# Optimization experiments

Measured on AMD Instinct MI355X. Metric: run time of the kernel, lower is better.

Reference implementation:

```python
import jax, jax.numpy as jnp
import numpy as np

OUT_FEATURES = 4096
IN_FEATURES = 4096
R = 16
DIST = 4
N_FREQ = 10000
SCALING = 150.0


def setup_inputs() -> dict:
    key = jax.random.key(0)
    k_x, k_w, k_b, k_s, k_a, k_i = jax.random.split(key, 6)
    x = jax.random.normal(k_x, (4, 2048, IN_FEATURES), dtype=jnp.float32)
    base_w = jax.random.normal(k_w, (OUT_FEATURES, IN_FEATURES), dtype=jnp.float32) * 0.02
    base_b = jax.random.normal(k_b, (OUT_FEATURES,), dtype=jnp.float32) * 0.02
    spectrum = jax.random.normal(k_s, (N_FREQ,), dtype=jnp.float32)
    hora_A = jax.random.normal(k_a, (R, IN_FEATURES), dtype=jnp.float32)
    # torch uses randperm(r*out_features)[:n_frequency] -> unique flat indices
    idx = jax.random.permutation(k_i, R * OUT_FEATURES)[:N_FREQ].astype(jnp.int32)
    return {"x": x, "base_w": base_w, "base_b": base_b,
            "spectrum": spectrum, "hora_A": hora_A, "idx": idx}


def reference(x, base_w, base_b, spectrum, hora_A, idx):
    # --- get_delta_weight ---
    rows = idx // R            # index into out_features
    cols = idx % R             # index into r
    dense_spectrum = jnp.zeros((OUT_FEATURES, R), dtype=spectrum.dtype)
    dense_spectrum = dense_spectrum.at[rows, cols].set(spectrum)
    # chunk_size = ceil(out/dist) = 1024; out divisible by dist -> pure reshape
    chunks = dense_spectrum.reshape(DIST, OUT_FEATURES // DIST, R)
    B = jnp.fft.ifft2(chunks, axes=(-2, -1)).real.astype(spectrum.dtype)
    B = B.reshape(OUT_FEATURES, R)
    delta_w = (B * SCALING) @ hora_A          # [out_features, in_features]
    # --- forward: base linear + adapter linear ---
    base_out = jnp.einsum('bsi,oi->bso', x, base_w) + base_b
    result = base_out + jnp.einsum('bsi,oi->bso', x, delta_w)
    return result
```

## Files before the change

### kernel.cpp

```cpp
#include <hip/hip_runtime.h>
#include <hip/hip_bf16.h>


#define OUTF 4096
#define INF  4096
#define NFREQ 10000
#define MDIM 8192
#define KT   (INF / 64)

typedef __attribute__((ext_vector_type(8))) short bf16x8;
typedef __attribute__((ext_vector_type(4))) float f32x4;

__device__ __forceinline__ unsigned int bf16pack2(float a, float b) {
    unsigned int ua = __builtin_bit_cast(unsigned int, a);
    unsigned int ub = __builtin_bit_cast(unsigned int, b);
    ua = (ua + 0x7fffu + ((ua >> 16) & 1u)) >> 16;
    ub = (ub + 0x7fffu + ((ub >> 16) & 1u)) & 0xffff0000u;
    return ua | ub;
}

__device__ __forceinline__ void async_copy16(const void* g, void* l) {
    __builtin_amdgcn_global_load_lds(
        (__attribute__((address_space(1))) void*)(g),
        (__attribute__((address_space(3))) void*)(l),
        16, 0, 0);
}

__global__ __launch_bounds__(256) void compact_kernel(
        const float* __restrict__ spectrum, const int* __restrict__ idx,
        int2* __restrict__ cjk, int* __restrict__ ccnt) {
    const int p   = blockIdx.x;
    const int tid = threadIdx.x;
    const int wv  = tid >> 6, ln = tid & 63;
    __shared__ int wcnt[4];
    int cnt = 0;
    for (int i0 = wv * 64; i0 < NFREQ; i0 += 256) {
        const int i = i0 + ln;
        bool m = (i < NFREQ) && ((idx[i] >> 14) == p);
        cnt += __popcll(__ballot(m));
    }
    if (ln == 0) wcnt[wv] = cnt;
    __syncthreads();
    int base = 0;
    for (int w = 0; w < wv; ++w) base += wcnt[w];
    for (int i0 = wv * 64; i0 < NFREQ; i0 += 256) {
        const int i = i0 + ln;
        bool m = false; int id = 0;
        if (i < NFREQ) { id = idx[i]; m = ((id >> 14) == p); }
        unsigned long long bal = __ballot(m);
        if (m) {
            int pos = base + __popcll(bal & ((1ull << ln) - 1ull));
            if (pos < 4096)
                cjk[p * 4096 + pos] =
                    make_int2(id & 16383, __builtin_bit_cast(int, spectrum[i]));
        }
        base += __popcll(bal);
    }
    if (tid == 0) {
        int t = wcnt[0] + wcnt[1] + wcnt[2] + wcnt[3];
        ccnt[p] = (t < 4096) ? t : 4096;
    }
}

__global__ __launch_bounds__(256) void buildB_kernel(
        const int2* __restrict__ cjk, const int* __restrict__ ccnt,
        float* __restrict__ Bout) {
    __shared__ int2  s_jkv[4096];
    __shared__ float s_part[4][64];
    const int tid  = threadIdx.x;
    const int gid0 = blockIdx.x * 64;
    const int p    = gid0 >> 14;
    const int cnt  = ccnt[p];
    for (int t = tid; t < cnt; t += 256) s_jkv[t] = cjk[p * 4096 + t];
    __syncthreads();
    const int qtr  = tid >> 6;
    const int ol   = tid & 63;
    const int gid  = gid0 + ol;
    const int o    = gid >> 4;
    const int r    = gid & 15;
    const int m    = o & 1023;
    const int qlen = (cnt + 3) >> 2;
    const int t0   = qtr * qlen;
    const int t1   = (t0 + qlen < cnt) ? t0 + qlen : cnt;
    const float c  = 6.283185307179586f / 16384.f;
    float acc = 0.f;
    for (int t = t0; t < t1; ++t) {
        const int2 jv = s_jkv[t];
        const int j = jv.x >> 4, k = jv.x & 15;
        int ph = (((j * m) & 1023) << 4) + (((k * r) & 15) << 10);
        acc += __builtin_bit_cast(float, jv.y) * __cosf((float)(ph & 16383) * c);
    }
    s_part[qtr][ol] = acc;
    __syncthreads();
    if (tid < 64) {
        float s = s_part[0][tid] + s_part[1][tid] + s_part[2][tid] + s_part[3][tid];
        Bout[gid0 + tid] = s * (150.f / 16384.f);
    }
}

__global__ __launch_bounds__(256) void build_w_kernel(
        const float* __restrict__ bw, const float* __restrict__ A,
        const float* __restrict__ Bs, unsigned short* __restrict__ W) {
    const int n0 = blockIdx.x * 8;
    __shared__ float sB[8][16];
    if (threadIdx.x < 128)
        ((float*)sB)[threadIdx.x] = Bs[n0 * 16 + threadIdx.x];
    __syncthreads();
    const float4* A4 = (const float4*)A;
    const float4* bw4 = (const float4*)bw;
    uint2* W2 = (uint2*)W;
#pragma unroll 1
    for (int q = 0; q < 4; ++q) {
        const int c4 = threadIdx.x + q * 256;
        float4 a[16];
#pragma unroll
        for (int r = 0; r < 16; ++r) a[r] = A4[r * 1024 + c4];
#pragma unroll 1
        for (int nn = 0; nn < 8; ++nn) {
            const int n = n0 + nn;
            float4 wv = bw4[n * 1024 + c4];
#pragma unroll
            for (int r = 0; r < 16; ++r) {
                float s = sB[nn][r];
                wv.x += s * a[r].x; wv.y += s * a[r].y;
                wv.z += s * a[r].z; wv.w += s * a[r].w;
            }
            W2[n * 1024 + c4] = make_uint2(bf16pack2(wv.x, wv.y),
                                           bf16pack2(wv.z, wv.w));
        }
    }
}

__global__ __launch_bounds__(256) void cvt_x_kernel(
        const float4* __restrict__ x, uint2* __restrict__ xb, int n4) {
    for (int i = blockIdx.x * blockDim.x + threadIdx.x; i < n4;
         i += gridDim.x * blockDim.x) {
        float4 v = x[i];
        xb[i] = make_uint2(bf16pack2(v.x, v.y), bf16pack2(v.z, v.w));
    }
}

__global__ __launch_bounds__(512, 2) void gemm256_kernel(
        const unsigned short* __restrict__ Xb,
        const unsigned short* __restrict__ Wb,
        const float* __restrict__ bias, float* __restrict__ C) {
    __shared__ __align__(1024) char lds[131072];

    const int tid  = threadIdx.x;
    const int lane = tid & 63;
    const int wid  = tid >> 6;
    const int wm   = wid >> 2;
    const int wn   = wid & 3;

    int bid = blockIdx.x;
    bid = (bid & 7) * 64 + (bid >> 3);
    const int tm = bid >> 4;
    const int tn = bid & 15;
    const int arow0 = tm * 256;
    const int brow0 = tn * 256;

    const int srow  = tid >> 3;
    const int scole = (((tid & 7) * 16) ^ ((srow & 7) << 4)) >> 1;
    const int sldsb = tid * 16;

    const int l15 = lane & 15;
    const int kx0 = ((lane >> 4) * 16) ^ ((lane & 7) << 4);
    const int kx1 = kx0 ^ 64;
    const int abase0 = (wm * 128 + l15) * 128;
    const int bbase0 = 32768 + (wn * 64 + l15) * 128;

    f32x4 acc[8][4] = {};
    bf16x8 af[4][2], bfa[2][2], bfb[2][2];

#define STAGE_HALF(mat, grow0, t, ldsbase) do {                               \
        const unsigned short* _s =                                            \
            (mat) + ((grow0) + srow) * INF + (t) * 64 + scole;                \
        async_copy16(_s, lds + (ldsbase) + sldsb);                            \
        async_copy16(_s + 64 * INF, lds + (ldsbase) + 8192 + sldsb);          \
    } while (0)

#define LDA(DB, m, kh) (*(const bf16x8*)(lds + (DB) + abase0 + (m) * 2048 + ((kh) ? kx1 : kx0)))
#define LDB(DB, n, kh) (*(const bf16x8*)(lds + (DB) + bbase0 + (n) * 2048 + ((kh) ? kx1 : kx0)))
#define MFMA(a, b, c) __builtin_amdgcn_mfma_f32_16x16x32_bf16((a), (b), (c), 0, 0, 0)
#define BARRIER() do { asm volatile("" ::: "memory");                         \
                       __builtin_amdgcn_s_barrier();                          \
                       asm volatile("" ::: "memory"); } while (0)
#define LGKM0()  asm volatile("s_waitcnt lgkmcnt(0)" ::: "memory")

#define QMFMA(mh, BF)                                                         \
    __builtin_amdgcn_s_setprio(1);                                            \
    _Pragma("unroll") for (int ks = 0; ks < 2; ++ks)                          \
        _Pragma("unroll") for (int m = 0; m < 4; ++m)                         \
            _Pragma("unroll") for (int n = 0; n < 2; ++n)                     \
                acc[(mh) * 4 + m][(BF) * 2 + n] =                             \
                    MFMA(af[m][ks], ((BF) ? bfb : bfa)[n][ks],                \
                         acc[(mh) * 4 + m][(BF) * 2 + n]);                    \
    __builtin_amdgcn_s_setprio(0)

#define RD_AF(DB, mh)                                                         \
    _Pragma("unroll") for (int m = 0; m < 4; ++m) {                           \
        af[m][0] = LDA(DB, (mh) * 4 + m, 0);                                  \
        af[m][1] = LDA(DB, (mh) * 4 + m, 1); }
#define RD_BFA(DB)                                                            \
    _Pragma("unroll") for (int n = 0; n < 2; ++n) {                           \
        bfa[n][0] = LDB(DB, n, 0); bfa[n][1] = LDB(DB, n, 1); }
#define RD_BFB(DB)                                                            \
    _Pragma("unroll") for (int n = 0; n < 2; ++n) {                           \
        bfb[n][0] = LDB(DB, n + 2, 0); bfb[n][1] = LDB(DB, n + 2, 1); }

#define PAIR(CUR, OTH, s) do {                                                \
                         \
    RD_AF(CUR, 0);                                                            \
    STAGE_HALF(Xb, arow0 + 128, (s) + 1, (OTH) + 16384);                      \
    BARRIER(); LGKM0(); QMFMA(0, 0); BARRIER();                               \
                        \
    RD_BFB(CUR);                                                              \
    STAGE_HALF(Wb, brow0 + 128, (s) + 1, (OTH) + 49152);                      \
    BARRIER(); LGKM0(); QMFMA(0, 1); BARRIER();                               \
                        \
    RD_AF(CUR, 1);                                                            \
    if ((s) + 2 < KT) STAGE_HALF(Wb, brow0, (s) + 2, (CUR) + 32768);          \
    BARRIER(); LGKM0(); QMFMA(1, 0); BARRIER();                               \
                \
    if ((s) + 2 < KT) {                                                       \
        STAGE_HALF(Xb, arow0, (s) + 2, (CUR) + 0);                            \
        asm volatile("s_waitcnt vmcnt(4)" ::: "memory");                      \
    } else { asm volatile("s_waitcnt vmcnt(0)" ::: "memory"); }               \
    BARRIER();                                                                \
    RD_BFA(OTH);                                                              \
    QMFMA(1, 1); BARRIER();                                                   \
                        \
    RD_AF(OTH, 0);                                                            \
    if ((s) + 2 < KT) STAGE_HALF(Xb, arow0 + 128, (s) + 2, (CUR) + 16384);    \
    BARRIER(); LGKM0(); QMFMA(0, 0); BARRIER();                               \
                       \
    RD_BFB(OTH);                                                              \
    if ((s) + 2 < KT) STAGE_HALF(Wb, brow0 + 128, (s) + 2, (CUR) + 49152);    \
    BARRIER(); LGKM0(); QMFMA(0, 1); BARRIER();                               \
                       \
    RD_AF(OTH, 1);                                                            \
    if ((s) + 3 < KT) STAGE_HALF(Wb, brow0, (s) + 3, (OTH) + 32768);          \
    BARRIER(); LGKM0(); QMFMA(1, 0); BARRIER();                               \
    \
    if ((s) + 3 < KT) {                                                       \
        STAGE_HALF(Xb, arow0, (s) + 3, (OTH) + 0);                            \
        asm volatile("s_waitcnt vmcnt(4)" ::: "memory");                      \
    } else { asm volatile("s_waitcnt vmcnt(0)" ::: "memory"); }               \
    BARRIER();                                                                \
    if ((s) + 2 < KT) { RD_BFA(CUR); }                                        \
    QMFMA(1, 1); BARRIER();                                                   \
} while (0)

    STAGE_HALF(Wb, brow0,       0, 32768);
    STAGE_HALF(Xb, arow0,       0, 0);
    STAGE_HALF(Xb, arow0 + 128, 0, 16384);
    STAGE_HALF(Wb, brow0 + 128, 0, 49152);
    STAGE_HALF(Wb, brow0,       1, 65536 + 32768);
    STAGE_HALF(Xb, arow0,       1, 65536 + 0);
    asm volatile("s_waitcnt vmcnt(4)" ::: "memory");
    BARRIER();
    RD_BFA(0);

    for (int s = 0; s < KT; s += 2)
        PAIR(0, 65536, s);

#pragma unroll
    for (int n = 0; n < 4; ++n) {
        const int gcol = brow0 + wn * 64 + n * 16 + l15;
        const float bv = bias[gcol];
#pragma unroll
        for (int m = 0; m < 8; ++m) {
            const int grow = arow0 + wm * 128 + m * 16 + (lane >> 4) * 4;
#pragma unroll
            for (int rg = 0; rg < 4; ++rg)
                C[(grow + rg) * OUTF + gcol] = acc[m][n][rg] + bv;
        }
    }
#undef STAGE_HALF
#undef LDA
#undef LDB
#undef MFMA
#undef BARRIER
#undef LGKM0
#undef QMFMA
#undef RD_AF
#undef RD_BFA
#undef RD_BFB
#undef PAIR
}

extern "C" void kernel_launch(void* const* d_in, const int* in_sizes, int n_in,
                              void* d_out, int out_size, void* d_ws, size_t ws_size,
                              hipStream_t stream) {
    const float* x    = (const float*)d_in[0];
    const float* bw   = (const float*)d_in[1];
    const float* bb   = (const float*)d_in[2];
    const float* spec = (const float*)d_in[3];
    const float* ha   = (const float*)d_in[4];
    const int*   idx  = (const int*)d_in[5];
    float* out = (float*)d_out;

    char* ws = (char*)d_ws;
    float*          Bbuf = (float*)ws;
    unsigned short* Wb   = (unsigned short*)(ws + 262144);
    unsigned short* Xb   = (unsigned short*)(ws + 262144 + 33554432);
    int2*           cjk  = (int2*)(ws + 262144 + 33554432 + 67108864);
    int*            ccnt = (int*)(ws + 262144 + 33554432 + 67108864 + 131072);

    compact_kernel<<<4, 256, 0, stream>>>(spec, idx, cjk, ccnt);
    buildB_kernel<<<1024, 256, 0, stream>>>(cjk, ccnt, Bbuf);
    build_w_kernel<<<512, 256, 0, stream>>>(bw, ha, Bbuf, Wb);
    cvt_x_kernel<<<2048, 256, 0, stream>>>((const float4*)x, (uint2*)Xb,
                                           (MDIM * INF) / 4);
    gemm256_kernel<<<512, 512, 0, stream>>>(Xb, Wb, bb, out);
}
```

Before: 405.4 us.

## Separable 2D inverse DFT via bucketing by column, fuse x conversion into B kernel

Replaces the direct per-element 2D inverse DFT over all nonzeros with a separable evaluation. The compact kernel now also sorts entries by frequency column k into buckets. The B kernel then does a 1024-point row transform per (m,k) and a 16-point column transform in shared memory, which cuts the trig and accumulate work roughly by a factor of 16. The x-to-bf16 conversion is merged into the same launch so the B build overlaps with the bandwidth-bound conversion and one kernel launch is dropped, at the cost of an uneven block workload.

New measurement: 388.1 us. 1.04x faster.

```diff
diff --git a/kernel.cpp b/kernel.cpp
--- a/kernel.cpp
+++ b/kernel.cpp
@@ -26,13 +26,17 @@
         16, 0, 0);
 }
 
-__global__ __launch_bounds__(256) void compact_kernel(
+__global__ __launch_bounds__(256) void compact_sort_kernel(
         const float* __restrict__ spectrum, const int* __restrict__ idx,
-        int2* __restrict__ cjk, int* __restrict__ ccnt) {
+        int2* __restrict__ cjk2, int* __restrict__ boff) {
     const int p   = blockIdx.x;
     const int tid = threadIdx.x;
     const int wv  = tid >> 6, ln = tid & 63;
-    __shared__ int wcnt[4];
+    __shared__ int2 s_list[4096];
+    __shared__ int  wcnt[4];
+    __shared__ int  s_cnt;
+    __shared__ int  kcnt[16];
+    __shared__ int  kbase[17];
     int cnt = 0;
     for (int i0 = wv * 64; i0 < NFREQ; i0 += 256) {
         const int i = i0 + ln;
@@ -51,50 +55,97 @@
         if (m) {
             int pos = base + __popcll(bal & ((1ull << ln) - 1ull));
             if (pos < 4096)
-                cjk[p * 4096 + pos] =
-                    make_int2(id & 16383, __builtin_bit_cast(int, spectrum[i]));
+                s_list[pos] = make_int2(id & 16383,
+                                        __builtin_bit_cast(int, spectrum[i]));
         }
         base += __popcll(bal);
     }
     if (tid == 0) {
         int t = wcnt[0] + wcnt[1] + wcnt[2] + wcnt[3];
-        ccnt[p] = (t < 4096) ? t : 4096;
-    }
-}
-
-__global__ __launch_bounds__(256) void buildB_kernel(
-        const int2* __restrict__ cjk, const int* __restrict__ ccnt,
-        float* __restrict__ Bout) {
-    __shared__ int2  s_jkv[4096];
-    __shared__ float s_part[4][64];
-    const int tid  = threadIdx.x;
-    const int gid0 = blockIdx.x * 64;
-    const int p    = gid0 >> 14;
-    const int cnt  = ccnt[p];
-    for (int t = tid; t < cnt; t += 256) s_jkv[t] = cjk[p * 4096 + t];
-    __syncthreads();
-    const int qtr  = tid >> 6;
-    const int ol   = tid & 63;
-    const int gid  = gid0 + ol;
-    const int o    = gid >> 4;
-    const int r    = gid & 15;
-    const int m    = o & 1023;
-    const int qlen = (cnt + 3) >> 2;
-    const int t0   = qtr * qlen;
-    const int t1   = (t0 + qlen < cnt) ? t0 + qlen : cnt;
-    const float c  = 6.283185307179586f / 16384.f;
-    float acc = 0.f;
-    for (int t = t0; t < t1; ++t) {
-        const int2 jv = s_jkv[t];
-        const int j = jv.x >> 4, k = jv.x & 15;
-        int ph = (((j * m) & 1023) << 4) + (((k * r) & 15) << 10);
-        acc += __builtin_bit_cast(float, jv.y) * __cosf((float)(ph & 16383) * c);
-    }
-    s_part[qtr][ol] = acc;
-    __syncthreads();
-    if (tid < 64) {
-        float s = s_part[0][tid] + s_part[1][tid] + s_part[2][tid] + s_part[3][tid];
-        Bout[gid0 + tid] = s * (150.f / 16384.f);
+        s_cnt = (t < 4096) ? t : 4096;
+    }
+    __syncthreads();
+    const int n = s_cnt;
+    for (int q = 0; q < 4; ++q) {
+        const int k = wv * 4 + q;
+        int c = 0;
+        for (int t0 = 0; t0 < n; t0 += 64) {
+            const int t = t0 + ln;
+            bool m = (t < n) && ((s_list[t].x & 15) == k);
+            c += __popcll(__ballot(m));
+        }
+        if (ln == 0) kcnt[k] = c;
+    }
+    __syncthreads();
+    if (tid == 0) {
+        int a = 0;
+        for (int k = 0; k < 16; ++k) { kbase[k] = a; a += kcnt[k]; }
+        kbase[16] = a;
+    }
+    __syncthreads();
+    for (int q = 0; q < 4; ++q) {
+        const int k = wv * 4 + q;
+        int b2 = kbase[k];
+        for (int t0 = 0; t0 < n; t0 += 64) {
+            const int t = t0 + ln;
+            bool m = (t < n) && ((s_list[t].x & 15) == k);
+            unsigned long long bal = __ballot(m);
+            if (m) {
+                int pos = b2 + __popcll(bal & ((1ull << ln) - 1ull));
+                cjk2[p * 4096 + pos] = make_int2(s_list[t].x >> 4, s_list[t].y);
+            }
+            b2 += __popcll(bal);
+        }
+    }
+    if (tid < 17) boff[p * 17 + tid] = kbase[tid];
+}
+
+__global__ __launch_bounds__(256) void buildB_cvt_kernel(
+        const int2* __restrict__ cjk2, const int* __restrict__ boff,
+        float* __restrict__ Bout,
+        const float4* __restrict__ x4, uint2* __restrict__ xb) {
+    __shared__ int2  s_jv[4096];
+    __shared__ float s1re[16][16];
+    __shared__ float s1im[16][17];
+    if (blockIdx.x < 256) {
+        const int tid  = threadIdx.x;
+        const int p    = blockIdx.x >> 6;
+        const int mblk = blockIdx.x & 63;
+        const int cnt  = boff[p * 17 + 16];
+        for (int t = tid; t < cnt; t += 256) s_jv[t] = cjk2[p * 4096 + t];
+        __syncthreads();
+        const int m_loc = tid >> 4;
+        const int k     = tid & 15;
+        const int m     = mblk * 16 + m_loc;
+        const int kb0   = boff[p * 17 + k];
+        const int kb1   = boff[p * 17 + k + 1];
+        const float c1  = 6.283185307179586f / 1024.f;
+        float re = 0.f, im = 0.f;
+        for (int t = kb0; t < kb1; ++t) {
+            const int2 jv = s_jv[t];
+            const float v = __builtin_bit_cast(float, jv.y);
+            const float ang = (float)((jv.x * m) & 1023) * c1;
+            re += v * __cosf(ang);
+            im += v * __sinf(ang);
+        }
+        s1re[m_loc][k] = re;
+        s1im[m_loc][k] = im;
+        __syncthreads();
+        const int r = k;
+        const float c2 = 6.283185307179586f / 16.f;
+        float b = 0.f;
+#pragma unroll
+        for (int k2 = 0; k2 < 16; ++k2) {
+            const float ang = (float)((k2 * r) & 15) * c2;
+            b += s1re[m_loc][k2] * __cosf(ang) - s1im[m_loc][k2] * __sinf(ang);
+        }
+        const int o = p * 1024 + m;
+        Bout[o * 16 + r] = b * (150.f / 16384.f);
+    }
+    const int n4 = (MDIM * INF) / 4;
+    for (int i = blockIdx.x * 256 + threadIdx.x; i < n4; i += 2048 * 256) {
+        float4 v = x4[i];
+        xb[i] = make_uint2(bf16pack2(v.x, v.y), bf16pack2(v.z, v.w));
     }
 }
 
@@ -128,15 +179,6 @@
             W2[n * 1024 + c4] = make_uint2(bf16pack2(wv.x, wv.y),
                                            bf16pack2(wv.z, wv.w));
         }
-    }
-}
-
-__global__ __launch_bounds__(256) void cvt_x_kernel(
-        const float4* __restrict__ x, uint2* __restrict__ xb, int n4) {
-    for (int i = blockIdx.x * blockDim.x + threadIdx.x; i < n4;
-         i += gridDim.x * blockDim.x) {
-        float4 v = x[i];
-        xb[i] = make_uint2(bf16pack2(v.x, v.y), bf16pack2(v.z, v.w));
     }
 }
 
@@ -304,13 +346,12 @@
     float*          Bbuf = (float*)ws;
     unsigned short* Wb   = (unsigned short*)(ws + 262144);
     unsigned short* Xb   = (unsigned short*)(ws + 262144 + 33554432);
-    int2*           cjk  = (int2*)(ws + 262144 + 33554432 + 67108864);
-    int*            ccnt = (int*)(ws + 262144 + 33554432 + 67108864 + 131072);
-
-    compact_kernel<<<4, 256, 0, stream>>>(spec, idx, cjk, ccnt);
-    buildB_kernel<<<1024, 256, 0, stream>>>(cjk, ccnt, Bbuf);
+    int2*           cjk2 = (int2*)(ws + 262144 + 33554432 + 67108864);
+    int*            boff = (int*)(ws + 262144 + 33554432 + 67108864 + 131072);
+
+    compact_sort_kernel<<<4, 256, 0, stream>>>(spec, idx, cjk2, boff);
+    buildB_cvt_kernel<<<2048, 256, 0, stream>>>(cjk2, boff, Bbuf,
+                                                (const float4*)x, (uint2*)Xb);
     build_w_kernel<<<512, 256, 0, stream>>>(bw, ha, Bbuf, Wb);
-    cvt_x_kernel<<<2048, 256, 0, stream>>>((const float4*)x, (uint2*)Xb,
-                                           (MDIM * INF) / 4);
     gemm256_kernel<<<512, 512, 0, stream>>>(Xb, Wb, bb, out);
 }
```
